# Kernel optimization log

Hardware: AMD Instinct MI355X
Metric: run time of the kernel (lower is better)

## Reference

```python
import jax, jax.numpy as jnp
import numpy as np

STEPS = 2
P_TOPP = 0.9
TAU = 1.0
LN_EPS = 1e-5


def _top_p_attention(pooled, W1, W2, W3):
    # pooled: (N, C). Bilinear scores -> softmax -> nucleus (top-p) sparsify -> renorm.
    e1 = pooled @ W1.T                      # (N, d)
    e3 = pooled @ W3.T                      # (N, d)
    logits = (e1 @ W2.T) @ e3.T / TAU       # (N, N)
    attn = jax.nn.softmax(logits, axis=-1)
    srt = jnp.sort(attn, axis=-1)[:, ::-1]  # descending
    csum = jnp.cumsum(srt, axis=-1)
    keep = (csum - srt) < P_TOPP            # keep entries whose exclusive cum-prob < p
    thr = jnp.min(jnp.where(keep, srt, jnp.inf), axis=-1, keepdims=True)
    masked = jnp.where(attn >= thr, attn, 0.0)
    return masked / jnp.clip(jnp.sum(masked, axis=-1, keepdims=True), 1e-12)


def _layernorm(h, gamma, beta):
    mu = jnp.mean(h, axis=-1, keepdims=True)
    var = jnp.mean(jnp.square(h - mu), axis=-1, keepdims=True)
    return (h - mu) * jax.lax.rsqrt(var + LN_EPS) * gamma + beta


def _forward(x, prior, W1, W2, W3, prior_fwd_w, adaptive_w, ln_gamma, ln_beta, alpha):
    # Row-normalised prior (forward diffusion operator)
    Rf = prior / jnp.clip(jnp.sum(prior, axis=1, keepdims=True), 1e-12)
    Xf = x
    Xa = x
    residual = jnp.zeros_like(x)
    for idx in range(STEPS):
        pooled = jnp.mean(Xa, axis=1)                      # protein axis pooling -> (N_P, C)
        attn = _top_p_attention(pooled, W1, W2, W3)        # (N_P, N_P)
        Xf = jnp.einsum('ij,jkc->ikc', Rf, Xf)
        Xa = jnp.einsum('ij,jkc->ikc', attn, Xa)
        delta = jnp.einsum('ikc,dc->ikd', Xf, prior_fwd_w[idx]) \
              + jnp.einsum('ikc,dc->ikd', Xa, adaptive_w[idx])
        residual = residual + delta                        # dropout is identity in eval mode
    gate = jax.nn.sigmoid(alpha)                           # (1,)
    return _layernorm(x + gate * residual, ln_gamma, ln_beta)


def setup_inputs() -> dict:
    key = jax.random.key(0)
    ks = jax.random.split(key, 8)
    N_P, N_C, C, D = 2048, 64, 128, 64
    x = jax.random.normal(ks[0], (N_P, N_C, C), dtype=jnp.float32)
    prior = jax.random.uniform(ks[1], (N_P, N_P), dtype=jnp.float32)
    W1 = jax.random.normal(ks[2], (D, C), dtype=jnp.float32) / np.sqrt(C)
    W2 = jax.random.normal(ks[3], (D, D), dtype=jnp.float32) / np.sqrt(D)
    W3 = jax.random.normal(ks[4], (D, C), dtype=jnp.float32) / np.sqrt(C)
    prior_fwd_w = jax.random.normal(ks[5], (STEPS, C, C), dtype=jnp.float32) / np.sqrt(C)
    adaptive_w = jax.random.normal(ks[6], (STEPS, C, C), dtype=jnp.float32) / np.sqrt(C)
    ln_gamma = jnp.ones((C,), dtype=jnp.float32)
    ln_beta = jnp.zeros((C,), dtype=jnp.float32)
    alpha = jnp.zeros((1,), dtype=jnp.float32)
    return {"x": x, "prior": prior, "W1": W1, "W2": W2, "W3": W3,
            "prior_fwd_w": prior_fwd_w, "adaptive_w": adaptive_w,
            "ln_gamma": ln_gamma, "ln_beta": ln_beta, "alpha": alpha}


def reference(x, prior, W1, W2, W3, prior_fwd_w, adaptive_w, ln_gamma, ln_beta, alpha):
    return _forward(x, prior, W1, W2, W3, prior_fwd_w, adaptive_w, ln_gamma, ln_beta, alpha)
```

## Files before the change

### kernel.cpp

```cpp
#include <hip/hip_runtime.h>

typedef unsigned short u16;
typedef __attribute__((ext_vector_type(8))) short short8;
typedef __attribute__((ext_vector_type(4))) float f32x4;
typedef __attribute__((ext_vector_type(16))) float f32x16;

#define AS1 __attribute__((address_space(1)))
#define AS3 __attribute__((address_space(3)))

__device__ __forceinline__ void async_cp16(const void* g, void* l) {
  __builtin_amdgcn_global_load_lds((const AS1 unsigned int*)g, (AS3 unsigned int*)l, 16, 0, 0);
}

__device__ __forceinline__ u16 f2bf(float f) {
  union { float f; unsigned u; } v; v.f = f;
  unsigned r = v.u + 0x7fffu + ((v.u >> 16) & 1u);
  return (u16)(r >> 16);
}
__device__ __forceinline__ float bf2f(u16 h) {
  union { unsigned u; float f; } v; v.u = ((unsigned)h) << 16;
  return v.f;
}

template<int MODE>
__global__ __launch_bounds__(512, 2) void gemm32(
    const u16* __restrict__ Aa, const u16* __restrict__ Ap,
    const u16* __restrict__ Ba, const u16* __restrict__ Bp,
    int N, int K,
    u16* __restrict__ Crow, int crow_ld,
    u16* __restrict__ Cta, u16* __restrict__ Ctp, int ct_ld)
{
  extern __shared__ u16 smem[];
  const int tid  = threadIdx.x;
  const int lane = tid & 63;
  const int w    = tid >> 6;
  const int half2 = blockIdx.y >> 3;
  const int m0 = (blockIdx.y & 7) * 256;
  const int n0 = blockIdx.x * 256;
  const u16* A = half2 ? Ap : Aa;
  const u16* B = half2 ? Bp : Ba;
  const int coloff = half2 * 128;
  const int wm = w >> 2;
  const int wn = w & 3;
  const int l31  = lane & 31;
  const int half = lane >> 5;
  const int pl   = (l31 & 3) ^ ((l31 >> 2) & 3);

  f32x16 acc[4][2];
#pragma unroll
  for (int i = 0; i < 4; i++)
#pragma unroll
    for (int j = 0; j < 2; j++)
#pragma unroll
      for (int r = 0; r < 16; r++) acc[i][j][r] = 0.f;

  const int sr4 = lane >> 2, sc4 = lane & 3;
  const int pp  = (sr4 & 3) ^ (sr4 >> 2);
  const int gko = (sc4 ^ pp) * 8;
  const u16* gA0 = A + (size_t)(m0 + w * 32 + sr4) * K + gko;
  const u16* gA1 = A + (size_t)(m0 + w * 32 + 16 + sr4) * K + gko;
  const u16* gB0 = B + (size_t)(n0 + w * 32 + sr4) * K + gko;
  const u16* gB1 = B + (size_t)(n0 + w * 32 + 16 + sr4) * K + gko;
  const int la = w * 1024;

#define ISSUE(tt) do {                                       \
    u16* sa = smem + ((tt) & 3) * 16384 + la;                \
    u16* sb = sa + 8192;                                     \
    const int ko = (tt) * 32;                                \
    async_cp16(gA0 + ko, sa); async_cp16(gA1 + ko, sa + 512);\
    async_cp16(gB0 + ko, sb); async_cp16(gB1 + ko, sb + 512);\
  } while (0)

  const int NT = K >> 5;
  ISSUE(0); ISSUE(1);
  asm volatile("s_waitcnt vmcnt(4)" ::: "memory");
  __builtin_amdgcn_s_barrier();

  for (int t = 0; t < NT; ++t) {
    const u16* sAp = smem + (t & 3) * 16384;
    const u16* sBp = sAp + 8192;
    const bool st = (t + 2 < NT);
    if (st) ISSUE(t + 2);

    const int ar = (wm * 128 + l31) * 32;
    const int br = (wn * 64 + l31) * 32;
    short8 Af[4][2], Bf[2][2];
#define FRAG(ks) ((((ks) * 2 + half) ^ pl) * 8)
#pragma unroll
    for (int i = 0; i < 4; i++)
#pragma unroll
      for (int ks = 0; ks < 2; ks++)
        Af[i][ks] = *(const short8*)(sAp + ar + i * 1024 + FRAG(ks));
#pragma unroll
    for (int j = 0; j < 2; j++)
#pragma unroll
      for (int ks = 0; ks < 2; ks++)
        Bf[j][ks] = *(const short8*)(sBp + br + j * 1024 + FRAG(ks));
#undef FRAG

    __builtin_amdgcn_s_setprio(1);
#pragma unroll
    for (int i = 0; i < 4; i++)
#pragma unroll
      for (int j = 0; j < 2; j++)
#pragma unroll
        for (int ks = 0; ks < 2; ks++)
          acc[i][j] = __builtin_amdgcn_mfma_f32_32x32x16_bf16(Af[i][ks], Bf[j][ks], acc[i][j], 0, 0, 0);
    __builtin_amdgcn_s_setprio(0);

    if (st) { asm volatile("s_waitcnt vmcnt(4)" ::: "memory"); }
    else    { asm volatile("s_waitcnt vmcnt(0)" ::: "memory"); }
    __builtin_amdgcn_s_barrier();
  }
#undef ISSUE

  u16* T = smem;

#pragma unroll
  for (int pr = 0; pr < 4; pr++) {
    if (wm == (pr >> 1)) {
#pragma unroll
      for (int ii = 0; ii < 2; ii++)
#pragma unroll
        for (int j = 0; j < 2; j++)
#pragma unroll
          for (int r = 0; r < 16; r++) {
            const int rloc = ii * 32 + (r & 3) + 8 * (r >> 2) + 4 * half;
            T[rloc * 264 + wn * 64 + j * 32 + l31] = f2bf(acc[(pr & 1) * 2 + ii][j][r]);
          }
    }
    __syncthreads();
    {
      const int row = tid >> 3, c8 = tid & 7;
      const size_t grow = (size_t)(m0 + pr * 64 + row);
      const size_t crow = grow * (size_t)(N >> 7) + (n0 >> 7) + (c8 >> 2);
      u16* dst = Crow + crow * (size_t)crow_ld + coloff + (c8 & 3) * 32;
      const u16* src = T + row * 264 + c8 * 32;
#pragma unroll
      for (int u = 0; u < 4; u++) ((float4*)dst)[u] = ((const float4*)src)[u];
    }
    __syncthreads();
  }

  if constexpr (MODE == 1) {
    u16* Ct = half2 ? Ctp : Cta;
#pragma unroll
    for (int p = 0; p < 4; p++) {
      if (wn == p) {
#pragma unroll
        for (int i = 0; i < 4; i++)
#pragma unroll
          for (int j = 0; j < 2; j++)
#pragma unroll
            for (int r = 0; r < 16; r++) {
              const int nloc = j * 32 + l31;
              const int mcol = wm * 128 + i * 32 + (r & 3) + 8 * (r >> 2) + 4 * half;
              T[nloc * 264 + mcol] = f2bf(acc[i][j][r]);
            }
      }
      __syncthreads();
      {
        const int row = tid >> 3, c8 = tid & 7;
        u16* dst = Ct + (size_t)(n0 + p * 64 + row) * ct_ld + m0 + c8 * 32;
        const u16* src = T + row * 264 + c8 * 32;
#pragma unroll
        for (int u = 0; u < 4; u++) ((float4*)dst)[u] = ((const float4*)src)[u];
      }
      __syncthreads();
    }
  }
}

template<int MODE>
__global__ __launch_bounds__(256) void gemm_bt(
    const u16* __restrict__ A, const u16* __restrict__ B,
    int M, int N, int K,
    float* __restrict__ Cf,
    u16* __restrict__ Crow, int crow_ld, int crow_coloff)
{
  extern __shared__ char smemc[];
  u16* sA = (u16*)smemc;
  u16* sB = (u16*)(smemc + 8192);
  const int tid  = threadIdx.x;
  const int lane = tid & 63;
  const int wid  = tid >> 6;
  const int m0 = blockIdx.y * 128;
  const int n0 = blockIdx.x * 128;
  const int wm = (wid >> 1) * 64;
  const int wn = (wid & 1) * 64;
  const int ml = lane & 15;
  const int qd = lane >> 4;
  const int qs = (qd ^ ((ml >> 1) & 3)) * 8;

  f32x4 acc[4][4];
  const f32x4 zero = {0.f, 0.f, 0.f, 0.f};
#pragma unroll
  for (int i = 0; i < 4; i++)
#pragma unroll
    for (int j = 0; j < 4; j++) acc[i][j] = zero;

  const int r4 = tid >> 2;
  const int pq = (r4 >> 1) & 3;
  const int c4 = ((tid & 3) ^ pq) * 8;
  const u16* gA0 = A + (size_t)(m0 + r4) * K + c4;
  const u16* gA1 = A + (size_t)(m0 + 64 + r4) * K + c4;
  const u16* gB0 = B + (size_t)(n0 + r4) * K + c4;
  const u16* gB1 = B + (size_t)(n0 + 64 + r4) * K + c4;
  u16* lA0 = sA + wid * 512;
  u16* lA1 = sA + 2048 + wid * 512;
  u16* lB0 = sB + wid * 512;
  u16* lB1 = sB + 2048 + wid * 512;

  for (int k0 = 0; k0 < K; k0 += 32) {
    async_cp16(gA0 + k0, lA0);
    async_cp16(gA1 + k0, lA1);
    async_cp16(gB0 + k0, lB0);
    async_cp16(gB1 + k0, lB1);
    __syncthreads();
    short8 af[4], bfr[4];
#pragma unroll
    for (int i = 0; i < 4; i++)
      af[i] = *(const short8*)(sA + (wm + i * 16 + ml) * 32 + qs);
#pragma unroll
    for (int j = 0; j < 4; j++)
      bfr[j] = *(const short8*)(sB + (wn + j * 16 + ml) * 32 + qs);
#pragma unroll
    for (int i = 0; i < 4; i++)
#pragma unroll
      for (int j = 0; j < 4; j++)
        acc[i][j] = __builtin_amdgcn_mfma_f32_16x16x32_bf16(af[i], bfr[j], acc[i][j], 0, 0, 0);
    __syncthreads();
  }

  if constexpr (MODE == 3) {
#pragma unroll
    for (int i = 0; i < 4; i++) {
      const int mr = m0 + wm + i * 16 + qd * 4;
#pragma unroll
      for (int j = 0; j < 4; j++) {
        const int nc = n0 + wn + j * 16 + ml;
        float* p = Cf + (size_t)mr * N + nc;
#pragma unroll
        for (int r = 0; r < 4; r++) p[(size_t)r * N] = acc[i][j][r];
      }
    }
  } else {
    u16* T = (u16*)smemc;
#pragma unroll
    for (int i = 0; i < 4; i++)
#pragma unroll
      for (int j = 0; j < 4; j++)
#pragma unroll
        for (int r = 0; r < 4; r++)
          T[(wm + i * 16 + qd * 4 + r) * 136 + wn + j * 16 + ml] = f2bf(acc[i][j][r]);
    __syncthreads();
    const int row = tid >> 1, halfr = tid & 1;
    const size_t crow = (size_t)(m0 + row) * (N >> 7) + (n0 >> 7);
    u16* dst = Crow + crow * (size_t)crow_ld + crow_coloff + halfr * 64;
    const u16* src = T + row * 136 + halfr * 64;
#pragma unroll
    for (int u = 0; u < 8; u++) ((float4*)dst)[u] = ((const float4*)src)[u];
  }
}

__global__ __launch_bounds__(256) void prep_k(
    const float* __restrict__ prior, ushort4* __restrict__ priorS,
    const float* __restrict__ x, u16* __restrict__ xt,
    const float* __restrict__ pw, const float* __restrict__ aw,
    u16* __restrict__ btc)
{
  const int bid = blockIdx.x;
  const int t = threadIdx.x;
  if (bid < 2048) {
    __shared__ float red[256];
    const int i = bid;
    const float* p = prior + (size_t)i * 2048;
    float s = 0.f;
    for (int j = t; j < 2048; j += 256) s += p[j];
    red[t] = s; __syncthreads();
    for (int o = 128; o; o >>= 1) { if (t < o) red[t] += red[t + o]; __syncthreads(); }
    const float inv = 1.0f / red[0];
    const float4* pv = (const float4*)p;
    ushort4* dv = priorS + (size_t)i * 512;
#pragma unroll
    for (int j = t; j < 512; j += 256) {
      const float4 v = pv[j];
      ushort4 o;
      o.x = f2bf(v.x * inv); o.y = f2bf(v.y * inv); o.z = f2bf(v.z * inv); o.w = f2bf(v.w * inv);
      dv[j] = o;
    }
  } else if (bid < 6144) {
    __shared__ float S[64][65];
    const int b2 = bid - 2048;
    const int n0 = (b2 & 127) * 64;
    const int j0 = (b2 >> 7) * 64;
    const int rr = t >> 4, cxc = (t & 15) * 4;
#pragma unroll
    for (int p = 0; p < 4; p++) {
      const float4 v = *(const float4*)(x + (size_t)(j0 + rr + p * 16) * 8192 + n0 + cxc);
      S[rr + p * 16][cxc + 0] = v.x; S[rr + p * 16][cxc + 1] = v.y;
      S[rr + p * 16][cxc + 2] = v.z; S[rr + p * 16][cxc + 3] = v.w;
    }
    __syncthreads();
    const int nl = t >> 2, ch = (t & 3) * 16;
    alignas(16) u16 tmp[16];
#pragma unroll
    for (int u = 0; u < 16; u++) tmp[u] = f2bf(S[ch + u][nl]);
    float4* dst = (float4*)(xt + (size_t)(n0 + nl) * 2048 + j0 + ch);
    dst[0] = ((const float4*)tmp)[0];
    dst[1] = ((const float4*)tmp)[1];
  } else {
    const int idx = (bid - 6144) * 256 + t;
    const int k = idx & 255, d = (idx >> 8) & 127, s = idx >> 15;
    const float v = (k < 128) ? aw[(s * 128 + d) * 128 + k] : pw[(s * 128 + d) * 128 + (k - 128)];
    btc[idx] = f2bf(v);
  }
}

template<int SRC>
__global__ __launch_bounds__(256) void pooled_epre_k(
    const float* __restrict__ xf, const u16* __restrict__ comb,
    const float* __restrict__ W1, const float* __restrict__ W2,
    const float* __restrict__ W3,
    u16* __restrict__ e3b, u16* __restrict__ fb)
{
  __shared__ float red[256];
  __shared__ float pr[128];
  __shared__ float e1s[64];
  const int i = blockIdx.x, t = threadIdx.x;
  const int c = t & 127, h = t >> 7;
  float s = 0.f;
  if constexpr (SRC == 0) {
    const float* base = xf + (size_t)i * 8192 + c;
    for (int k = h * 32; k < h * 32 + 32; k++) s += base[(size_t)k * 128];
  } else {
    const u16* base = comb + (size_t)i * 64 * 256 + c;
    for (int k = h * 32; k < h * 32 + 32; k++) s += bf2f(base[(size_t)k * 256]);
  }
  red[t] = s; __syncthreads();
  if (t < 128) pr[t] = (red[t] + red[t + 128]) * (1.f / 64.f);
  __syncthreads();
  if (t < 128) {
    const float* Wm = (t < 64) ? W1 : W3;
    const int d = t & 63;
    float sv = 0.f;
    for (int cc = 0; cc < 128; cc++) sv += pr[cc] * Wm[d * 128 + cc];
    if (t < 64) e1s[d] = sv;
    else        e3b[i * 64 + d] = f2bf(sv);
  }
  __syncthreads();
  if (t < 64) {
    float sf = 0.f;
    for (int dd = 0; dd < 64; dd++) sf += e1s[dd] * W2[t * 64 + dd];
    fb[i * 64 + t] = f2bf(sf);
  }
}

__device__ __forceinline__ float waveRedSum(float v) {
#pragma unroll
  for (int o = 1; o < 64; o <<= 1) v += __shfl_xor(v, o);
  return __shfl(v, 0);
}
__device__ __forceinline__ float waveRedMax(float v) {
#pragma unroll
  for (int o = 1; o < 64; o <<= 1) v = fmaxf(v, __shfl_xor(v, o));
  return __shfl(v, 0);
}

__global__ __launch_bounds__(256) void topp_k(const float* __restrict__ logits,
                                              u16* __restrict__ attnb) {
  const int w = threadIdx.x >> 6, l = threadIdx.x & 63;
  const int i = blockIdx.x * 4 + w;
  const float4* row = (const float4*)(logits + (size_t)i * 2048);
  float E[32];
  float mx = -1e30f;
#pragma unroll
  for (int k = 0; k < 8; k++) {
    const float4 v = row[k * 64 + l];
    E[k * 4 + 0] = v.x; E[k * 4 + 1] = v.y; E[k * 4 + 2] = v.z; E[k * 4 + 3] = v.w;
    mx = fmaxf(fmaxf(mx, fmaxf(v.x, v.y)), fmaxf(v.z, v.w));
  }
  mx = waveRedMax(mx);
  float S = 0.f;
#pragma unroll
  for (int u = 0; u < 32; u++) { E[u] = __expf(E[u] - mx); S += E[u]; }
  S = waveRedSum(S);
  const float target = 0.9f * S;
  float lo = 0.f, hi = 1.f;
  for (int it = 0; it < 32; ++it) {
    const float mid = 0.5f * (lo + hi);
    float g = 0.f;
#pragma unroll
    for (int u = 0; u < 32; u++) g += (E[u] > mid) ? E[u] : 0.f;
    g = waveRedSum(g);
    const bool below = (g < target);
    hi = below ? mid : hi;
    lo = below ? lo : mid;
  }
  float Sk = 0.f;
#pragma unroll
  for (int u = 0; u < 32; u++) Sk += (E[u] > lo) ? E[u] : 0.f;
  Sk = waveRedSum(Sk);
  const float inv = 1.f / Sk;
  u16* dst = attnb + (size_t)i * 2048;
#pragma unroll
  for (int k = 0; k < 8; k++) {
    ushort4 o;
    o.x = f2bf(E[k * 4 + 0] > lo ? E[k * 4 + 0] * inv : 0.f);
    o.y = f2bf(E[k * 4 + 1] > lo ? E[k * 4 + 1] * inv : 0.f);
    o.z = f2bf(E[k * 4 + 2] > lo ? E[k * 4 + 2] * inv : 0.f);
    o.w = f2bf(E[k * 4 + 3] > lo ? E[k * 4 + 3] * inv : 0.f);
    *(ushort4*)(dst + k * 256 + l * 4) = o;
  }
}

__global__ void ln_k(const float* __restrict__ x,
                     const u16* __restrict__ d1, const u16* __restrict__ d2,
                     float* __restrict__ out,
                     const float* __restrict__ gamma, const float* __restrict__ beta,
                     const float* __restrict__ alpha) {
  const int wid = threadIdx.x >> 6, lane = threadIdx.x & 63;
  const float gate = 1.f / (1.f + expf(-alpha[0]));
  const float2 g = ((const float2*)gamma)[lane];
  const float2 b = ((const float2*)beta)[lane];
#pragma unroll
  for (int rr = 0; rr < 2; ++rr) {
    const size_t row = (size_t)blockIdx.x * 8 + wid * 2 + rr;
    const float2 xv = ((const float2*)(x + row * 128))[lane];
    const ushort2 r1 = ((const ushort2*)(d1 + row * 128))[lane];
    const ushort2 r2 = ((const ushort2*)(d2 + row * 128))[lane];
    const float h0 = xv.x + gate * (bf2f(r1.x) + bf2f(r2.x));
    const float h1 = xv.y + gate * (bf2f(r1.y) + bf2f(r2.y));
    float s = h0 + h1;
#pragma unroll
    for (int o = 32; o; o >>= 1) s += __shfl_down(s, o);
    const float mu = __shfl(s, 0) * (1.f / 128.f);
    const float d0 = h0 - mu, dd1 = h1 - mu;
    float vs = d0 * d0 + dd1 * dd1;
#pragma unroll
    for (int o = 32; o; o >>= 1) vs += __shfl_down(vs, o);
    const float rstd = rsqrtf(__shfl(vs, 0) * (1.f / 128.f) + 1e-5f);
    float2* op = (float2*)(out + row * 128);
    float2 ov;
    ov.x = d0 * rstd * g.x + b.x;
    ov.y = dd1 * rstd * g.y + b.y;
    op[lane] = ov;
  }
}

extern "C" void kernel_launch(void* const* d_in, const int* in_sizes, int n_in,
                              void* d_out, int out_size, void* d_ws, size_t ws_size,
                              hipStream_t stream) {
  const float* x     = (const float*)d_in[0];
  const float* prior = (const float*)d_in[1];
  const float* W1    = (const float*)d_in[2];
  const float* W2    = (const float*)d_in[3];
  const float* W3    = (const float*)d_in[4];
  const float* Pw    = (const float*)d_in[5];
  const float* Aw    = (const float*)d_in[6];
  const float* gamma = (const float*)d_in[7];
  const float* beta  = (const float*)d_in[8];
  const float* alpha = (const float*)d_in[9];
  float* out = (float*)d_out;

  char* w = (char*)d_ws;
  u16*   Xt_x   = (u16*)(w);
  u16*   XtA    = (u16*)(w + 33554432);
  u16*   XtF    = (u16*)(w + 67108864);
  u16*   comb   = (u16*)(w + 100663296);
  u16*   priorS = (u16*)(w + 167772160);
  u16*   attnb  = (u16*)(w + 176160768);
  u16*   e3b    = (u16*)(w + 185597952);
  u16*   fb     = (u16*)(w + 186122240);
  u16*   btc    = (u16*)(w + 186654720);
  float* logits1 = (float*)(w + 33554432);
  float* logits2 = (float*)(w);
  u16*   d1      = (u16*)(w);
  u16*   d2      = (u16*)(w + 33554432);
  (void)in_sizes; (void)n_in; (void)ws_size;

  static bool attr_done = false;
  if (!attr_done) {
    hipFuncSetAttribute(reinterpret_cast<const void*>(gemm32<1>),
                        hipFuncAttributeMaxDynamicSharedMemorySize, 131072);
    hipFuncSetAttribute(reinterpret_cast<const void*>(gemm32<2>),
                        hipFuncAttributeMaxDynamicSharedMemorySize, 131072);
    attr_done = true;
  }

  prep_k<<<6400, 256, 0, stream>>>(prior, (ushort4*)priorS, x, Xt_x, Pw, Aw, btc);

  pooled_epre_k<0><<<2048, 256, 0, stream>>>(x, nullptr, W1, W2, W3, e3b, fb);
  gemm_bt<3> <<<dim3(16, 16), 256, 16384, stream>>>(fb, e3b, 2048, 2048, 64,
                                                    logits1, nullptr, 0, 0);
  topp_k     <<<512, 256, 0, stream>>>(logits1, attnb);

  gemm32<1><<<dim3(32, 16), 512, 131072, stream>>>(attnb, priorS, Xt_x, Xt_x,
                                                   8192, 2048, comb, 256,
                                                   XtA, XtF, 2048);

  pooled_epre_k<1><<<2048, 256, 0, stream>>>(nullptr, comb, W1, W2, W3, e3b, fb);
  gemm_bt<3> <<<dim3(16, 16), 256, 16384, stream>>>(fb, e3b, 2048, 2048, 64,
                                                    logits2, nullptr, 0, 0);
  topp_k     <<<512, 256, 0, stream>>>(logits2, attnb);

  gemm_bt<2><<<dim3(1, 1024), 256, 34816, stream>>>(comb, btc, 131072, 128, 256,
                                                    nullptr, d1, 128, 0);

  gemm32<2><<<dim3(32, 16), 512, 131072, stream>>>(attnb, priorS, XtA, XtF,
                                                   8192, 2048, comb, 256,
                                                   nullptr, nullptr, 0);

  gemm_bt<2><<<dim3(1, 1024), 256, 34816, stream>>>(comb, btc + 32768, 131072, 128, 256,
                                                    nullptr, d2, 128, 0);

  ln_k<<<16384, 256, 0, stream>>>(x, d1, d2, out, gamma, beta, alpha);
}
```

Measured before the change: 636.2 us.

## Fuse final step projection GEMM with residual gate and layernorm

Replaces the last projection GEMM and the separate layernorm kernel with one kernel. It computes the step-2 delta tile in registers, stages it as bf16 in shared memory, then adds x, gated d1 and delta and applies layernorm per row. This avoids writing d2 to global memory, reading it back, and one kernel launch. In exchange it uses a new hand-written GEMM without double buffering and a single-pass variance formula, which is less numerically stable.

```diff
diff --git a/kernel.cpp b/kernel.cpp
--- a/kernel.cpp
+++ b/kernel.cpp
@@ -263,6 +263,117 @@
   }
 }
 
+__global__ __launch_bounds__(256) void gemm_ln(
+    const u16* __restrict__ A, const u16* __restrict__ Bm,
+    const float* __restrict__ x, const u16* __restrict__ d1,
+    const float* __restrict__ gamma, const float* __restrict__ beta,
+    const float* __restrict__ alpha, float* __restrict__ out)
+{
+  extern __shared__ char smemc[];
+  u16* sA = (u16*)smemc;
+  u16* sB = (u16*)(smemc + 8192);
+  const int tid  = threadIdx.x;
+  const int lane = tid & 63;
+  const int wid  = tid >> 6;
+  const int m0 = blockIdx.x * 128;
+  const int K = 256;
+  const int wm = (wid >> 1) * 64;
+  const int wn = (wid & 1) * 64;
+  const int ml = lane & 15;
+  const int qd = lane >> 4;
+  const int qs = (qd ^ ((ml >> 1) & 3)) * 8;
+
+  f32x4 acc[4][4];
+  const f32x4 zero = {0.f, 0.f, 0.f, 0.f};
+#pragma unroll
+  for (int i = 0; i < 4; i++)
+#pragma unroll
+    for (int j = 0; j < 4; j++) acc[i][j] = zero;
+
+  const int r4 = tid >> 2;
+  const int pq = (r4 >> 1) & 3;
+  const int c4 = ((tid & 3) ^ pq) * 8;
+  const u16* gA0 = A + (size_t)(m0 + r4) * K + c4;
+  const u16* gA1 = A + (size_t)(m0 + 64 + r4) * K + c4;
+  const u16* gB0 = Bm + (size_t)r4 * K + c4;
+  const u16* gB1 = Bm + (size_t)(64 + r4) * K + c4;
+  u16* lA0 = sA + wid * 512;
+  u16* lA1 = sA + 2048 + wid * 512;
+  u16* lB0 = sB + wid * 512;
+  u16* lB1 = sB + 2048 + wid * 512;
+
+  for (int k0 = 0; k0 < K; k0 += 32) {
+    async_cp16(gA0 + k0, lA0);
+    async_cp16(gA1 + k0, lA1);
+    async_cp16(gB0 + k0, lB0);
+    async_cp16(gB1 + k0, lB1);
+    __syncthreads();
+    short8 af[4], bfr[4];
+#pragma unroll
+    for (int i = 0; i < 4; i++)
+      af[i] = *(const short8*)(sA + (wm + i * 16 + ml) * 32 + qs);
+#pragma unroll
+    for (int j = 0; j < 4; j++)
+      bfr[j] = *(const short8*)(sB + (wn + j * 16 + ml) * 32 + qs);
+#pragma unroll
+    for (int i = 0; i < 4; i++)
+#pragma unroll
+      for (int j = 0; j < 4; j++)
+        acc[i][j] = __builtin_amdgcn_mfma_f32_16x16x32_bf16(af[i], bfr[j], acc[i][j], 0, 0, 0);
+    __syncthreads();
+  }
+
+  u16* T = (u16*)smemc;
+#pragma unroll
+  for (int i = 0; i < 4; i++)
+#pragma unroll
+    for (int j = 0; j < 4; j++)
+#pragma unroll
+      for (int r = 0; r < 4; r++)
+        T[(wm + i * 16 + qd * 4 + r) * 138 + wn + j * 16 + ml] = f2bf(acc[i][j][r]);
+  __syncthreads();
+
+  const int row = tid >> 1, hf = tid & 1;
+  const size_t grow = (size_t)m0 + row;
+  const float gate = 1.f / (1.f + expf(-alpha[0]));
+  const float4*  xp = (const float4*)(x + grow * 128 + hf * 64);
+  const ushort4* dp = (const ushort4*)(d1 + grow * 128 + hf * 64);
+  const ushort4* tp = (const ushort4*)(T + row * 138 + hf * 64);
+  float s = 0.f, s2 = 0.f;
+#pragma unroll 4
+  for (int u = 0; u < 16; u++) {
+    const float4 xv = xp[u];
+    const ushort4 dv = dp[u];
+    const ushort4 tv = tp[u];
+    const float h0 = xv.x + gate * (bf2f(dv.x) + bf2f(tv.x));
+    const float h1 = xv.y + gate * (bf2f(dv.y) + bf2f(tv.y));
+    const float h2 = xv.z + gate * (bf2f(dv.z) + bf2f(tv.z));
+    const float h3 = xv.w + gate * (bf2f(dv.w) + bf2f(tv.w));
+    s  += h0 + h1 + h2 + h3;
+    s2 += h0 * h0 + h1 * h1 + h2 * h2 + h3 * h3;
+  }
+  s  += __shfl_xor(s, 1);
+  s2 += __shfl_xor(s2, 1);
+  const float mu = s * (1.f / 128.f);
+  const float rstd = rsqrtf(s2 * (1.f / 128.f) - mu * mu + 1e-5f);
+  const float4* gp = (const float4*)(gamma + hf * 64);
+  const float4* bp = (const float4*)(beta + hf * 64);
+  float4* op = (float4*)(out + grow * 128 + hf * 64);
+#pragma unroll 4
+  for (int u = 0; u < 16; u++) {
+    const float4 xv = xp[u];
+    const ushort4 dv = dp[u];
+    const ushort4 tv = tp[u];
+    const float4 g = gp[u], b = bp[u];
+    float4 o;
+    o.x = (xv.x + gate * (bf2f(dv.x) + bf2f(tv.x)) - mu) * rstd * g.x + b.x;
+    o.y = (xv.y + gate * (bf2f(dv.y) + bf2f(tv.y)) - mu) * rstd * g.y + b.y;
+    o.z = (xv.z + gate * (bf2f(dv.z) + bf2f(tv.z)) - mu) * rstd * g.z + b.z;
+    o.w = (xv.w + gate * (bf2f(dv.w) + bf2f(tv.w)) - mu) * rstd * g.w + b.w;
+    op[u] = o;
+  }
+}
+
 __global__ __launch_bounds__(256) void prep_k(
     const float* __restrict__ prior, ushort4* __restrict__ priorS,
     const float* __restrict__ x, u16* __restrict__ xt,
@@ -414,40 +525,6 @@
   }
 }
 
-__global__ void ln_k(const float* __restrict__ x,
-                     const u16* __restrict__ d1, const u16* __restrict__ d2,
-                     float* __restrict__ out,
-                     const float* __restrict__ gamma, const float* __restrict__ beta,
-                     const float* __restrict__ alpha) {
-  const int wid = threadIdx.x >> 6, lane = threadIdx.x & 63;
-  const float gate = 1.f / (1.f + expf(-alpha[0]));
-  const float2 g = ((const float2*)gamma)[lane];
-  const float2 b = ((const float2*)beta)[lane];
-#pragma unroll
-  for (int rr = 0; rr < 2; ++rr) {
-    const size_t row = (size_t)blockIdx.x * 8 + wid * 2 + rr;
-    const float2 xv = ((const float2*)(x + row * 128))[lane];
-    const ushort2 r1 = ((const ushort2*)(d1 + row * 128))[lane];
-    const ushort2 r2 = ((const ushort2*)(d2 + row * 128))[lane];
-    const float h0 = xv.x + gate * (bf2f(r1.x) + bf2f(r2.x));
-    const float h1 = xv.y + gate * (bf2f(r1.y) + bf2f(r2.y));
-    float s = h0 + h1;
-#pragma unroll
-    for (int o = 32; o; o >>= 1) s += __shfl_down(s, o);
-    const float mu = __shfl(s, 0) * (1.f / 128.f);
-    const float d0 = h0 - mu, dd1 = h1 - mu;
-    float vs = d0 * d0 + dd1 * dd1;
-#pragma unroll
-    for (int o = 32; o; o >>= 1) vs += __shfl_down(vs, o);
-    const float rstd = rsqrtf(__shfl(vs, 0) * (1.f / 128.f) + 1e-5f);
-    float2* op = (float2*)(out + row * 128);
-    float2 ov;
-    ov.x = d0 * rstd * g.x + b.x;
-    ov.y = dd1 * rstd * g.y + b.y;
-    op[lane] = ov;
-  }
-}
-
 extern "C" void kernel_launch(void* const* d_in, const int* in_sizes, int n_in,
                               void* d_out, int out_size, void* d_ws, size_t ws_size,
                               hipStream_t stream) {
@@ -476,7 +553,6 @@
   float* logits1 = (float*)(w + 33554432);
   float* logits2 = (float*)(w);
   u16*   d1      = (u16*)(w);
-  u16*   d2      = (u16*)(w + 33554432);
   (void)in_sizes; (void)n_in; (void)ws_size;
 
   static bool attr_done = false;
@@ -511,8 +587,6 @@
                                                    8192, 2048, comb, 256,
                                                    nullptr, nullptr, 0);
 
-  gemm_bt<2><<<dim3(1, 1024), 256, 34816, stream>>>(comb, btc + 32768, 131072, 128, 256,
-                                                    nullptr, d2, 128, 0);
-
-  ln_k<<<16384, 256, 0, stream>>>(x, d1, d2, out, gamma, beta, alpha);
-}
+  gemm_ln<<<1024, 256, 35328, stream>>>(comb, btc + 32768, x, d1,
+                                        gamma, beta, alpha, out);
+}
```

Measured after the change: 683.4 us. 1.07x slower.

## Restructure gemm32 main loop into 8-wave quadrant pipeline with 16x16 MFMAs

Applied to the files above, without the earlier changes.

Rewrites the gemm32 inner loop to use 64-wide K tiles, double-buffered in shared memory, and splits each tile's work into four quadrant MFMA phases. The async global-to-LDS loads for the next tile are interleaved between those phases, with barriers after each one. It also switches from 32x32x16 to 16x16x32 bf16 MFMA with a new swizzled LDS layout, and updates the epilogue writes to match. The aim is to hide load latency behind MFMA work and cut LDS bank conflicts, at the cost of more barriers and more register pressure.

```diff
diff --git a/kernel.cpp b/kernel.cpp
--- a/kernel.cpp
+++ b/kernel.cpp
@@ -3,7 +3,6 @@
 typedef unsigned short u16;
 typedef __attribute__((ext_vector_type(8))) short short8;
 typedef __attribute__((ext_vector_type(4))) float f32x4;
-typedef __attribute__((ext_vector_type(16))) float f32x16;
 
 #define AS1 __attribute__((address_space(1)))
 #define AS3 __attribute__((address_space(3)))
@@ -40,94 +39,134 @@
   const u16* A = half2 ? Ap : Aa;
   const u16* B = half2 ? Bp : Ba;
   const int coloff = half2 * 128;
-  const int wm = w >> 2;
-  const int wn = w & 3;
-  const int l31  = lane & 31;
-  const int half = lane >> 5;
-  const int pl   = (l31 & 3) ^ ((l31 >> 2) & 3);
-
-  f32x16 acc[4][2];
-#pragma unroll
-  for (int i = 0; i < 4; i++)
-#pragma unroll
-    for (int j = 0; j < 2; j++)
-#pragma unroll
-      for (int r = 0; r < 16; r++) acc[i][j][r] = 0.f;
-
-  const int sr4 = lane >> 2, sc4 = lane & 3;
-  const int pp  = (sr4 & 3) ^ (sr4 >> 2);
-  const int gko = (sc4 ^ pp) * 8;
-  const u16* gA0 = A + (size_t)(m0 + w * 32 + sr4) * K + gko;
-  const u16* gA1 = A + (size_t)(m0 + w * 32 + 16 + sr4) * K + gko;
-  const u16* gB0 = B + (size_t)(n0 + w * 32 + sr4) * K + gko;
-  const u16* gB1 = B + (size_t)(n0 + w * 32 + 16 + sr4) * K + gko;
-  const int la = w * 1024;
-
-#define ISSUE(tt) do {                                       \
-    u16* sa = smem + ((tt) & 3) * 16384 + la;                \
-    u16* sb = sa + 8192;                                     \
-    const int ko = (tt) * 32;                                \
-    async_cp16(gA0 + ko, sa); async_cp16(gA1 + ko, sa + 512);\
-    async_cp16(gB0 + ko, sb); async_cp16(gB1 + ko, sb + 512);\
+  const int wm2 = w >> 2;
+  const int wn4 = w & 3;
+  const int nh  = wn4 >> 1;
+  const int nsub = (wn4 & 1) * 64;
+  const int ml = lane & 15;
+  const int qd = lane >> 4;
+  const int qs = (qd ^ ((ml >> 1) & 3)) * 8;
+
+  f32x4 acc[8][4];
+  const f32x4 zero = {0.f, 0.f, 0.f, 0.f};
+#pragma unroll
+  for (int i = 0; i < 8; i++)
+#pragma unroll
+    for (int j = 0; j < 4; j++) acc[i][j] = zero;
+
+  const int sr  = lane >> 2;
+  const int gch = ((lane & 3) ^ ((lane >> 3) & 3)) * 8;
+
+#define ST_A(tt, hh) do {                                                     \
+    u16* d0_ = smem + ((tt) & 1) * 32768 + ((hh) * 2 + 0) * 4096 + w * 512;   \
+    u16* d1_ = smem + ((tt) & 1) * 32768 + ((hh) * 2 + 1) * 4096 + w * 512;   \
+    const u16* s_ = A + (size_t)(m0 + (hh) * 128 + w * 16 + sr) * K + (tt) * 64 + gch; \
+    async_cp16(s_, d0_); async_cp16(s_ + 32, d1_);                            \
   } while (0)
-
-  const int NT = K >> 5;
-  ISSUE(0); ISSUE(1);
+#define ST_B(tt, hhn) do {                                                    \
+    u16* d0_ = smem + ((tt) & 1) * 32768 + 16384 + ((hhn) * 2 + 0) * 4096 + w * 512; \
+    u16* d1_ = smem + ((tt) & 1) * 32768 + 16384 + ((hhn) * 2 + 1) * 4096 + w * 512; \
+    const u16* s_ = B + (size_t)(n0 + (hhn) * 128 + w * 16 + sr) * K + (tt) * 64 + gch; \
+    async_cp16(s_, d0_); async_cp16(s_ + 32, d1_);                            \
+  } while (0)
+
+  short8 Af[4][2], Bf[2][2][2];
+
+#define READA(dbase, mq) do {                                                 \
+    _Pragma("unroll")                                                         \
+    for (int i_ = 0; i_ < 4; i_++)                                            \
+      _Pragma("unroll")                                                       \
+      for (int ks_ = 0; ks_ < 2; ks_++)                                       \
+        Af[i_][ks_] = *(const short8*)(smem + (dbase) + (wm2 * 2 + ks_) * 4096 \
+            + ((mq) * 64 + i_ * 16 + ml) * 32 + qs);                          \
+  } while (0)
+#define READB(dbase, nq) do {                                                 \
+    _Pragma("unroll")                                                         \
+    for (int jf_ = 0; jf_ < 2; jf_++)                                         \
+      _Pragma("unroll")                                                       \
+      for (int ks_ = 0; ks_ < 2; ks_++)                                       \
+        Bf[nq][jf_][ks_] = *(const short8*)(smem + (dbase) + 16384            \
+            + (nh * 2 + ks_) * 4096 + (nsub + (nq) * 32 + jf_ * 16 + ml) * 32 + qs); \
+  } while (0)
+#define MFMAQ(mq, nq) do {                                                    \
+    __builtin_amdgcn_s_setprio(1);                                            \
+    _Pragma("unroll")                                                         \
+    for (int i_ = 0; i_ < 4; i_++)                                            \
+      _Pragma("unroll")                                                       \
+      for (int jf_ = 0; jf_ < 2; jf_++)                                       \
+        _Pragma("unroll")                                                     \
+        for (int ks_ = 0; ks_ < 2; ks_++)                                     \
+          acc[(mq) * 4 + i_][(nq) * 2 + jf_] = __builtin_amdgcn_mfma_f32_16x16x32_bf16( \
+              Af[i_][ks_], Bf[nq][jf_][ks_], acc[(mq) * 4 + i_][(nq) * 2 + jf_], 0, 0, 0); \
+    __builtin_amdgcn_s_setprio(0);                                            \
+  } while (0)
+
+  const int NTI = K >> 7;
+  ST_B(0, 0); ST_B(0, 1); ST_A(0, 0); ST_A(0, 1); ST_B(1, 0); ST_B(1, 1);
   asm volatile("s_waitcnt vmcnt(4)" ::: "memory");
   __builtin_amdgcn_s_barrier();
 
-  for (int t = 0; t < NT; ++t) {
-    const u16* sAp = smem + (t & 3) * 16384;
-    const u16* sBp = sAp + 8192;
-    const bool st = (t + 2 < NT);
-    if (st) ISSUE(t + 2);
-
-    const int ar = (wm * 128 + l31) * 32;
-    const int br = (wn * 64 + l31) * 32;
-    short8 Af[4][2], Bf[2][2];
-#define FRAG(ks) ((((ks) * 2 + half) ^ pl) * 8)
-#pragma unroll
-    for (int i = 0; i < 4; i++)
-#pragma unroll
-      for (int ks = 0; ks < 2; ks++)
-        Af[i][ks] = *(const short8*)(sAp + ar + i * 1024 + FRAG(ks));
-#pragma unroll
-    for (int j = 0; j < 2; j++)
-#pragma unroll
-      for (int ks = 0; ks < 2; ks++)
-        Bf[j][ks] = *(const short8*)(sBp + br + j * 1024 + FRAG(ks));
-#undef FRAG
-
-    __builtin_amdgcn_s_setprio(1);
-#pragma unroll
-    for (int i = 0; i < 4; i++)
-#pragma unroll
-      for (int j = 0; j < 2; j++)
-#pragma unroll
-        for (int ks = 0; ks < 2; ks++)
-          acc[i][j] = __builtin_amdgcn_mfma_f32_32x32x16_bf16(Af[i][ks], Bf[j][ks], acc[i][j], 0, 0, 0);
-    __builtin_amdgcn_s_setprio(0);
-
+  for (int j = 0; j < NTI; ++j) {
+    const int T = 2 * j;
+    const bool st = (j + 1 < NTI);
+    const int b0 = (T & 1) ? 32768 : 0;
+    const int b1 = b0 ^ 32768;
+
+    READA(b0, 0); READB(b0, 0);
+    ST_A(T + 1, 0);
+    MFMAQ(0, 0);
+    __builtin_amdgcn_s_barrier();
+    READB(b0, 1);
+    ST_A(T + 1, 1);
+    MFMAQ(0, 1);
+    __builtin_amdgcn_s_barrier();
+    READA(b0, 1);
+    if (st) ST_B(T + 2, 0);
+    MFMAQ(1, 1);
+    __builtin_amdgcn_s_barrier();
+    if (st) ST_B(T + 2, 1);
+    MFMAQ(1, 0);
     if (st) { asm volatile("s_waitcnt vmcnt(4)" ::: "memory"); }
     else    { asm volatile("s_waitcnt vmcnt(0)" ::: "memory"); }
     __builtin_amdgcn_s_barrier();
-  }
-#undef ISSUE
+    READA(b1, 0); READB(b1, 0);
+    if (st) ST_A(T + 2, 0);
+    MFMAQ(0, 0);
+    __builtin_amdgcn_s_barrier();
+    READB(b1, 1);
+    if (st) ST_A(T + 2, 1);
+    MFMAQ(0, 1);
+    __builtin_amdgcn_s_barrier();
+    READA(b1, 1);
+    if (st) ST_B(T + 3, 0);
+    MFMAQ(1, 1);
+    __builtin_amdgcn_s_barrier();
+    if (st) ST_B(T + 3, 1);
+    MFMAQ(1, 0);
+    if (st) { asm volatile("s_waitcnt vmcnt(4)" ::: "memory"); }
+    else    { asm volatile("s_waitcnt vmcnt(0)" ::: "memory"); }
+    __builtin_amdgcn_s_barrier();
+  }
+#undef ST_A
+#undef ST_B
+#undef READA
+#undef READB
+#undef MFMAQ
 
   u16* T = smem;
 
 #pragma unroll
   for (int pr = 0; pr < 4; pr++) {
-    if (wm == (pr >> 1)) {
-#pragma unroll
-      for (int ii = 0; ii < 2; ii++)
-#pragma unroll
-        for (int j = 0; j < 2; j++)
-#pragma unroll
-          for (int r = 0; r < 16; r++) {
-            const int rloc = ii * 32 + (r & 3) + 8 * (r >> 2) + 4 * half;
-            T[rloc * 264 + wn * 64 + j * 32 + l31] = f2bf(acc[(pr & 1) * 2 + ii][j][r]);
-          }
+    if (wm2 == (pr >> 1)) {
+      const int mq = pr & 1;
+#pragma unroll
+      for (int i = 0; i < 4; i++)
+#pragma unroll
+        for (int nj = 0; nj < 4; nj++)
+#pragma unroll
+          for (int r = 0; r < 4; r++)
+            T[(i * 16 + qd * 4 + r) * 264 + wn4 * 64 + nj * 16 + ml] =
+                f2bf(acc[mq * 4 + i][nj][r]);
     }
     __syncthreads();
     {
@@ -146,16 +185,16 @@
     u16* Ct = half2 ? Ctp : Cta;
 #pragma unroll
     for (int p = 0; p < 4; p++) {
-      if (wn == p) {
-#pragma unroll
-        for (int i = 0; i < 4; i++)
-#pragma unroll
-          for (int j = 0; j < 2; j++)
-#pragma unroll
-            for (int r = 0; r < 16; r++) {
-              const int nloc = j * 32 + l31;
-              const int mcol = wm * 128 + i * 32 + (r & 3) + 8 * (r >> 2) + 4 * half;
-              T[nloc * 264 + mcol] = f2bf(acc[i][j][r]);
+      if (wn4 == p) {
+#pragma unroll
+        for (int mi = 0; mi < 8; mi++)
+#pragma unroll
+          for (int nj = 0; nj < 4; nj++)
+#pragma unroll
+            for (int r = 0; r < 4; r++) {
+              const int nloc = nj * 16 + ml;
+              const int mcol = wm2 * 128 + (mi >> 2) * 64 + (mi & 3) * 16 + qd * 4 + r;
+              T[nloc * 264 + mcol] = f2bf(acc[mi][nj][r]);
             }
       }
       __syncthreads();
```

Measured after the change: 583.3 us. -8.3%, faster.
